# Performance work log

Measured on AMD Instinct MI355X. Metric: run time of the kernel, lower is better.

Reference implementation:

```python
import jax, jax.numpy as jnp
import numpy as np

D = 256
NH = 8
DH = D // NH
DFF = 1024
NLAYER = 6
LIN = 20
HOUT = 10
NEG = -1e9


def _ln(x, s, b, eps=1e-5):
    mu = jnp.mean(x, axis=-1, keepdims=True)
    var = jnp.mean((x - mu) ** 2, axis=-1, keepdims=True)
    return (x - mu) * jax.lax.rsqrt(var + eps) * s + b


def setup_inputs() -> dict:
    key = jax.random.key(0)
    ks = jax.random.split(key, 24)
    B, C, Q = 2, 1536, 512
    sc = 0.02
    inp = {
        'ctx_x': jax.random.normal(ks[0], (B, C, LIN), jnp.float32),
        'ctx_z': jax.random.normal(ks[1], (B, C, HOUT), jnp.float32),
        'qry_x': jax.random.normal(ks[2], (B, Q, LIN), jnp.float32),
        't_ctx': jax.random.randint(ks[3], (B, C), 0, 1024, jnp.int64 if jax.config.jax_enable_x64 else jnp.int32),
        't_qry': jax.random.randint(ks[4], (B, Q), 0, 2048, jnp.int64 if jax.config.jax_enable_x64 else jnp.int32),
        'W_ctx': sc * jax.random.normal(ks[5], (D, LIN + HOUT), jnp.float32),
        'b_ctx': jnp.zeros((D,), jnp.float32),
        'W_qry': sc * jax.random.normal(ks[6], (D, LIN + HOUT), jnp.float32),
        'b_qry': jnp.zeros((D,), jnp.float32),
        'alpha': 0.01 * jnp.ones((NH,), jnp.float32),
        'Wqkv': sc * jax.random.normal(ks[7], (NLAYER, 3 * D, D), jnp.float32),
        'bqkv': jnp.zeros((NLAYER, 3 * D), jnp.float32),
        'Wo': sc * jax.random.normal(ks[8], (NLAYER, D, D), jnp.float32),
        'bo': jnp.zeros((NLAYER, D), jnp.float32),
        'ln1_s': jnp.ones((NLAYER, D), jnp.float32),
        'ln1_b': jnp.zeros((NLAYER, D), jnp.float32),
        'W1': sc * jax.random.normal(ks[9], (NLAYER, DFF, D), jnp.float32),
        'b1': jnp.zeros((NLAYER, DFF), jnp.float32),
        'W2': sc * jax.random.normal(ks[10], (NLAYER, D, DFF), jnp.float32),
        'b2': jnp.zeros((NLAYER, D), jnp.float32),
        'ln2_s': jnp.ones((NLAYER, D), jnp.float32),
        'ln2_b': jnp.zeros((NLAYER, D), jnp.float32),
        'W_out': sc * jax.random.normal(ks[11], (HOUT, D), jnp.float32),
        'b_out': jnp.zeros((HOUT,), jnp.float32),
    }
    return inp


def _forward(ctx_x, ctx_z, qry_x, t_ctx, t_qry, W_ctx, b_ctx, W_qry, b_qry,
             alpha, Wqkv, bqkv, Wo, bo, ln1_s, ln1_b, W1, b1, W2, b2,
             ln2_s, ln2_b, W_out, b_out):
    B, C, _ = ctx_x.shape
    Q = qry_x.shape[1]
    S = C + Q
    ctx_in = jnp.concatenate([ctx_x, ctx_z], axis=-1)               # [B,C,L+H]
    qry_in = jnp.concatenate([qry_x, jnp.zeros((B, Q, HOUT), ctx_x.dtype)], axis=-1)
    Z = jnp.concatenate([ctx_in @ W_ctx.T + b_ctx,
                         qry_in @ W_qry.T + b_qry], axis=1)          # [B,S,d]
    t_all = jnp.concatenate([t_ctx, t_qry], axis=1)                  # [B,S]
    # structural mask: nobody attends to query columns (True = disallowed)
    struct = (jnp.arange(S)[None, :] >= C)                           # [1,S] -> broadcast over rows
    nofuture = t_all[:, :, None] < t_all[:, None, :]                 # [B,S,S]
    mask = struct[None, :, :] | nofuture                             # [B,S,S]
    # learnable per-head recency bias: -alpha_h * |t_i - t_j|
    dist = jnp.abs(t_all[:, :, None] - t_all[:, None, :]).astype(Z.dtype)
    bias = -alpha[None, :, None, None] * dist[:, None, :, :]         # [B,h,S,S]
    scale = 1.0 / np.sqrt(DH)

    for l in range(NLAYER):
        qkv = Z @ Wqkv[l].T + bqkv[l]                                # [B,S,3d]
        q, k, v = jnp.split(qkv, 3, axis=-1)
        q = q.reshape(B, S, NH, DH).transpose(0, 2, 1, 3)            # [B,h,S,dh]
        k = k.reshape(B, S, NH, DH).transpose(0, 2, 1, 3)
        v = v.reshape(B, S, NH, DH).transpose(0, 2, 1, 3)
        scores = jnp.einsum('bhid,bhjd->bhij', q, k) * scale + bias
        scores = jnp.where(mask[:, None, :, :], NEG, scores)
        p = jax.nn.softmax(scores, axis=-1)
        attn = jnp.einsum('bhij,bhjd->bhid', p, v)                   # [B,h,S,dh]
        attn = attn.transpose(0, 2, 1, 3).reshape(B, S, D)
        Z = _ln(Z + attn @ Wo[l].T + bo[l], ln1_s[l], ln1_b[l])
        ff = jax.nn.relu(Z @ W1[l].T + b1[l]) @ W2[l].T + b2[l]
        Z = _ln(Z + ff, ln2_s[l], ln2_b[l])

    return Z[:, C:, :] @ W_out.T + b_out                             # [B,Q,H]


def reference(ctx_x, ctx_z, qry_x, t_ctx, t_qry, W_ctx, b_ctx, W_qry, b_qry,
              alpha, Wqkv, bqkv, Wo, bo, ln1_s, ln1_b, W1, b1, W2, b2,
              ln2_s, ln2_b, W_out, b_out):
    return _forward(ctx_x, ctx_z, qry_x, t_ctx, t_qry, W_ctx, b_ctx, W_qry,
                    b_qry, alpha, Wqkv, bqkv, Wo, bo, ln1_s, ln1_b, W1, b1,
                    W2, b2, ln2_s, ln2_b, W_out, b_out)
```

## Files before the change

kernel.cpp:

```cpp
#include <hip/hip_runtime.h>
#include <hip/hip_bf16.h>
#include <cstddef>

#define BB   2
#define CTX  1536
#define QQ   512
#define S_LEN 2048
#define DD   256
#define NH   8
#define DH   32
#define DFF  1024
#define NL   6
#define LIN  20
#define HOUTD 10
#define KHALF (CTX / 2)

typedef _Float16 f16x2 __attribute__((ext_vector_type(2)));
typedef _Float16 f16x4 __attribute__((ext_vector_type(4)));
typedef _Float16 f16x8 __attribute__((ext_vector_type(8)));
typedef float f32x4 __attribute__((ext_vector_type(4)));

#define N4_QKV (NL * 3 * DD * DD / 4)
#define N4_WO  (NL * DD * DD / 4)
#define N4_W1  (NL * DFF * DD / 4)
#define N4_W2  (NL * DD * DFF / 4)

__global__ __launch_bounds__(256) void cvtall_k(
    const float* __restrict__ wqkv, const float* __restrict__ wo,
    const float* __restrict__ w1, const float* __restrict__ w2,
    _Float16* __restrict__ hqkv, _Float16* __restrict__ ho,
    _Float16* __restrict__ h1, _Float16* __restrict__ h2)
{
    int i = blockIdx.x * 256 + threadIdx.x;
    const float* s; _Float16* t; int j = i;
    if (j < N4_QKV) { s = wqkv; t = hqkv; }
    else if ((j -= N4_QKV) < N4_WO) { s = wo; t = ho; }
    else if ((j -= N4_WO) < N4_W1) { s = w1; t = h1; }
    else if ((j -= N4_W1) < N4_W2) { s = w2; t = h2; }
    else return;
    float4 v = ((const float4*)s)[j];
    f16x4 h = {(_Float16)v.x, (_Float16)v.y, (_Float16)v.z, (_Float16)v.w};
    ((f16x4*)t)[j] = h;
}

__global__ __launch_bounds__(256) void embed_k(
    const float* __restrict__ ctx_x, const float* __restrict__ ctx_z,
    const float* __restrict__ qry_x,
    const float* __restrict__ W_ctx, const float* __restrict__ b_ctx,
    const float* __restrict__ W_qry, const float* __restrict__ b_qry,
    const int* __restrict__ t_ctx, const int* __restrict__ t_qry,
    float* __restrict__ Z, _Float16* __restrict__ Zh, float* __restrict__ tf)
{
    int row = blockIdx.x;
    int d = threadIdx.x;
    int b = row >> 11, s = row & (S_LEN - 1);
    float acc;
    if (s < CTX) {
        const float* x1 = ctx_x + (size_t)(b * CTX + s) * LIN;
        const float* x2 = ctx_z + (size_t)(b * CTX + s) * HOUTD;
        const float* w = W_ctx + (size_t)d * (LIN + HOUTD);
        acc = b_ctx[d];
        #pragma unroll
        for (int i = 0; i < LIN; i++) acc += x1[i] * w[i];
        #pragma unroll
        for (int i = 0; i < HOUTD; i++) acc += x2[i] * w[LIN + i];
        if (d == 0) tf[row] = (float)t_ctx[b * CTX + s];
    } else {
        int qi = s - CTX;
        const float* x1 = qry_x + (size_t)(b * QQ + qi) * LIN;
        const float* w = W_qry + (size_t)d * (LIN + HOUTD);
        acc = b_qry[d];
        #pragma unroll
        for (int i = 0; i < LIN; i++) acc += x1[i] * w[i];
        if (d == 0) tf[row] = (float)t_qry[b * QQ + qi];
    }
    Z[(size_t)row * DD + d] = acc;
    Zh[(size_t)row * DD + d] = (_Float16)acc;
}

__global__ __launch_bounds__(256) void hgemm_k(
    const _Float16* __restrict__ X, const _Float16* __restrict__ W,
    const float* __restrict__ bias, float* __restrict__ Y,
    float* __restrict__ Ysplit, _Float16* __restrict__ Yh,
    int M, int N, int K, int lda, int mode,
    _Float16* __restrict__ Qh, _Float16* __restrict__ Kh, _Float16* __restrict__ Vh)
{
    __shared__ _Float16 Ah[2][64][40];
    __shared__ _Float16 Bh[2][64][40];
    const int tid = threadIdx.x;
    const int bm = blockIdx.x << 6, bn = blockIdx.y << 6;
    const int kbase = blockIdx.z * K;
    const int lr = tid >> 2;
    const int lk = (tid & 3) << 3;
    const int w = tid >> 6, lane = tid & 63;
    const int c = lane & 15, g = lane >> 4;
    const int wm = (w >> 1) << 5, wn = (w & 1) << 5;

    f32x4 acc00 = {0.f,0.f,0.f,0.f}, acc01 = {0.f,0.f,0.f,0.f};
    f32x4 acc10 = {0.f,0.f,0.f,0.f}, acc11 = {0.f,0.f,0.f,0.f};

    const _Float16* Xp = X + (size_t)(bm + lr) * lda + kbase + lk;
    const _Float16* Wp = W + (size_t)(bn + lr) * lda + kbase + lk;

    f16x8 xa = *(const f16x8*)Xp;
    f16x8 wb = *(const f16x8*)Wp;
    const int nt = K >> 5;
    int buf = 0;
    for (int t = 0; t < nt; t++) {
        *(f16x8*)&Ah[buf][lr][lk] = xa;
        *(f16x8*)&Bh[buf][lr][lk] = wb;
        __syncthreads();
        if (t + 1 < nt) {
            xa = *(const f16x8*)(Xp + ((size_t)(t + 1) << 5));
            wb = *(const f16x8*)(Wp + ((size_t)(t + 1) << 5));
        }
        f16x8 a0 = *(const f16x8*)&Ah[buf][wm + c][g << 3];
        f16x8 a1 = *(const f16x8*)&Ah[buf][wm + 16 + c][g << 3];
        f16x8 b0 = *(const f16x8*)&Bh[buf][wn + c][g << 3];
        f16x8 b1 = *(const f16x8*)&Bh[buf][wn + 16 + c][g << 3];
        acc00 = __builtin_amdgcn_mfma_f32_16x16x32_f16(a0, b0, acc00, 0, 0, 0);
        acc01 = __builtin_amdgcn_mfma_f32_16x16x32_f16(a0, b1, acc01, 0, 0, 0);
        acc10 = __builtin_amdgcn_mfma_f32_16x16x32_f16(a1, b0, acc10, 0, 0, 0);
        acc11 = __builtin_amdgcn_mfma_f32_16x16x32_f16(a1, b1, acc11, 0, 0, 0);
        buf ^= 1;
    }

    float* Yt = blockIdx.z ? Ysplit : Y;
    f32x4 accs[2][2] = {{acc00, acc01}, {acc10, acc11}};
    #pragma unroll
    for (int fm = 0; fm < 2; fm++) {
        #pragma unroll
        for (int fn = 0; fn < 2; fn++) {
            int colb = bn + wn + (fn << 4) + c;
            float bv = (blockIdx.z == 0) ? bias[colb] : 0.0f;
            #pragma unroll
            for (int r = 0; r < 4; r++) {
                int row = bm + wm + (fm << 4) + (g << 2) + r;
                float v = accs[fm][fn][r] + bv;
                if (mode == 0) {
                    Yt[(size_t)row * N + colb] = v;
                } else if (mode == 1) {
                    Yh[(size_t)row * N + colb] = (_Float16)fmaxf(v, 0.0f);
                } else {
                    int which = colb >> 8, h = (colb >> 5) & 7, d = colb & 31;
                    int bb2 = row >> 11, ss = row & (S_LEN - 1);
                    int bhi = (bb2 << 3) + h;
                    _Float16 hv = (_Float16)v;
                    if (which == 0)      Qh[((size_t)bhi * S_LEN + ss) * DH + d] = hv;
                    else if (which == 1) Kh[((size_t)bhi * S_LEN + ss) * DH + d] = hv;
                    else                 Vh[((size_t)bhi * DH + d) * S_LEN + ss] = hv;
                }
            }
        }
    }
}

__global__ __launch_bounds__(256) void gemmln_k(
    const _Float16* __restrict__ X, const _Float16* __restrict__ W,
    const float* __restrict__ bias, float* __restrict__ Z,
    _Float16* __restrict__ Zh, const float* __restrict__ sw,
    const float* __restrict__ bw)
{
    __shared__ _Float16 Ast[2][16][40];
    __shared__ _Float16 Bst[2][256][40];
    __shared__ float lred[4][16][2];
    const int tid = threadIdx.x;
    const int bm = blockIdx.x << 4;
    const int w = tid >> 6, lane = tid & 63;
    const int c = lane & 15, g = lane >> 4;
    const int br = tid >> 2, bk = (tid & 3) << 3;

    f32x4 acc[4] = {};
    const _Float16* Wp = W + (size_t)br * DD + bk;
    f16x8 p0 = *(const f16x8*)Wp;
    f16x8 p1 = *(const f16x8*)(Wp + (size_t)64 * DD);
    f16x8 p2 = *(const f16x8*)(Wp + (size_t)128 * DD);
    f16x8 p3 = *(const f16x8*)(Wp + (size_t)192 * DD);
    f16x8 xa;
    if (tid < 64) xa = *(const f16x8*)(X + (size_t)(bm + br) * DD + bk);
    int buf = 0;
    #pragma unroll
    for (int t = 0; t < 8; t++) {
        if (tid < 64) *(f16x8*)&Ast[buf][br][bk] = xa;
        *(f16x8*)&Bst[buf][br][bk] = p0;
        *(f16x8*)&Bst[buf][br + 64][bk] = p1;
        *(f16x8*)&Bst[buf][br + 128][bk] = p2;
        *(f16x8*)&Bst[buf][br + 192][bk] = p3;
        __syncthreads();
        if (t < 7) {
            int o = (t + 1) << 5;
            if (tid < 64) xa = *(const f16x8*)(X + (size_t)(bm + br) * DD + o + bk);
            p0 = *(const f16x8*)(Wp + o);
            p1 = *(const f16x8*)(Wp + (size_t)64 * DD + o);
            p2 = *(const f16x8*)(Wp + (size_t)128 * DD + o);
            p3 = *(const f16x8*)(Wp + (size_t)192 * DD + o);
        }
        f16x8 a = *(const f16x8*)&Ast[buf][c][g << 3];
        #pragma unroll
        for (int f = 0; f < 4; f++) {
            f16x8 bfr = *(const f16x8*)&Bst[buf][(w << 6) + (f << 4) + c][g << 3];
            acc[f] = __builtin_amdgcn_mfma_f32_16x16x32_f16(a, bfr, acc[f], 0, 0, 0);
        }
        buf ^= 1;
    }

    float vals[4][4];
    float s1[4] = {0.f,0.f,0.f,0.f}, s2[4] = {0.f,0.f,0.f,0.f};
    #pragma unroll
    for (int f = 0; f < 4; f++) {
        int col = (w << 6) + (f << 4) + c;
        float bv = bias[col];
        #pragma unroll
        for (int r = 0; r < 4; r++) {
            int row = bm + (g << 2) + r;
            float v = acc[f][r] + bv + Z[(size_t)row * DD + col];
            vals[f][r] = v; s1[r] += v; s2[r] += v * v;
        }
    }
    #pragma unroll
    for (int off = 1; off < 16; off <<= 1) {
        #pragma unroll
        for (int r = 0; r < 4; r++) {
            s1[r] += __shfl_xor(s1[r], off, 64);
            s2[r] += __shfl_xor(s2[r], off, 64);
        }
    }
    if (c == 0) {
        #pragma unroll
        for (int r = 0; r < 4; r++) {
            lred[w][(g << 2) + r][0] = s1[r];
            lred[w][(g << 2) + r][1] = s2[r];
        }
    }
    __syncthreads();
    float mu_r[4], rs_r[4];
    #pragma unroll
    for (int r = 0; r < 4; r++) {
        int lr_ = (g << 2) + r;
        float S1 = lred[0][lr_][0] + lred[1][lr_][0] + lred[2][lr_][0] + lred[3][lr_][0];
        float S2 = lred[0][lr_][1] + lred[1][lr_][1] + lred[2][lr_][1] + lred[3][lr_][1];
        float mu = S1 * (1.0f / 256.0f);
        float var = S2 * (1.0f / 256.0f) - mu * mu;
        mu_r[r] = mu; rs_r[r] = rsqrtf(var + 1e-5f);
    }
    #pragma unroll
    for (int f = 0; f < 4; f++) {
        int col = (w << 6) + (f << 4) + c;
        float swv = sw[col], bwv = bw[col];
        #pragma unroll
        for (int r = 0; r < 4; r++) {
            int row = bm + (g << 2) + r;
            float o = (vals[f][r] - mu_r[r]) * rs_r[r] * swv + bwv;
            Z[(size_t)row * DD + col] = o;
            Zh[(size_t)row * DD + col] = (_Float16)o;
        }
    }
}

__global__ __launch_bounds__(256) void ln4_k(
    float* __restrict__ Z, const float* __restrict__ Y0,
    const float* __restrict__ Y1,
    const float* __restrict__ sw, const float* __restrict__ bw,
    _Float16* __restrict__ Zh)
{
    const int w = threadIdx.x >> 6, lane = threadIdx.x & 63;
    const int row = (blockIdx.x << 2) + w;
    float4 z = ((const float4*)(Z + (size_t)row * DD))[lane];
    float4 y = ((const float4*)(Y0 + (size_t)row * DD))[lane];
    float4 y2 = ((const float4*)(Y1 + (size_t)row * DD))[lane];
    float x0 = z.x + y.x + y2.x, x1 = z.y + y.y + y2.y;
    float x2 = z.z + y.z + y2.z, x3 = z.w + y.w + y2.w;
    float s1 = (x0 + x1) + (x2 + x3);
    float s2 = (x0 * x0 + x1 * x1) + (x2 * x2 + x3 * x3);
    #pragma unroll
    for (int off = 1; off < 64; off <<= 1) {
        s1 += __shfl_xor(s1, off, 64);
        s2 += __shfl_xor(s2, off, 64);
    }
    float mu = s1 * (1.0f / 256.0f);
    float var = s2 * (1.0f / 256.0f) - mu * mu;
    float rs = rsqrtf(var + 1e-5f);
    float4 sv = ((const float4*)sw)[lane];
    float4 bv = ((const float4*)bw)[lane];
    float o0 = (x0 - mu) * rs * sv.x + bv.x;
    float o1 = (x1 - mu) * rs * sv.y + bv.y;
    float o2 = (x2 - mu) * rs * sv.z + bv.z;
    float o3 = (x3 - mu) * rs * sv.w + bv.w;
    ((float4*)(Z + (size_t)row * DD))[lane] = make_float4(o0, o1, o2, o3);
    f16x4 oh = {(_Float16)o0, (_Float16)o1, (_Float16)o2, (_Float16)o3};
    ((f16x4*)(Zh + (size_t)row * DD))[lane] = oh;
}

__global__ __launch_bounds__(1024, 4) void attn_k(
    const _Float16* __restrict__ Qf, const _Float16* __restrict__ Kf,
    const _Float16* __restrict__ Vf, const float* __restrict__ tf_all,
    const float* __restrict__ alpha, _Float16* __restrict__ O)
{
    const int bh = blockIdx.x >> 4;
    const int itile = blockIdx.x & 15;
    const int b = bh >> 3, h = bh & 7;
    const int tid = threadIdx.x;
    const int w16 = tid >> 6;
    const int wg = w16 >> 3;
    const int wq = w16 & 7;
    const int ltid = tid & 511;
    const int lane = tid & 63;
    const int c = lane & 15, g = lane >> 4;
    const int i0 = (itile << 7) + (wq << 4);
    const int jbase = wg * KHALF;

    __shared__ __align__(16) char smem[38912];
    _Float16 (*Kl)[2][64][40] = (_Float16(*)[2][64][40])smem;
    _Float16 (*Vl)[2][32][72] = (_Float16(*)[2][32][72])(smem + 20480);
    float (*sacc)[16][36] = (float(*)[16][36])smem;
    float (*sml)[2][16] = (float(*)[2][16])(smem + 36864);

    const float LOG2E = 1.44269504088896f;
    const float sc2 = 0.17677669529663687f * LOG2E;
    const float ah2 = alpha[h] * LOG2E;

    const _Float16* Qbh = Qf + (size_t)bh * S_LEN * DH;
    const _Float16* Kbh = Kf + (size_t)bh * S_LEN * DH;
    const _Float16* Vbh = Vf + (size_t)bh * DH * S_LEN;
    const float* tb = tf_all + b * S_LEN;

    f16x8 qfrag = *(const f16x8*)(Qbh + (size_t)(i0 + c) * DH + (g << 3));
    const float ti = tb[i0 + c];

    const int lh = ltid & 255;
    const int kr = lh >> 2, kc = (lh & 3) << 3;
    const int vr = lh >> 3, vc = (lh & 7) << 3;
    const bool doK = (ltid < 256);

    float m2 = -3.0e38f, l = 0.0f;
    f32x4 acc0 = {0.f, 0.f, 0.f, 0.f};
    f32x4 acc1 = {0.f, 0.f, 0.f, 0.f};
    const f32x4 zero = {0.f, 0.f, 0.f, 0.f};

    f16x8 pre;
    if (doK) pre = *(const f16x8*)(Kbh + (size_t)(jbase + kr) * DH + kc);
    else     pre = *(const f16x8*)(Vbh + (size_t)vr * S_LEN + jbase + vc);
    int buf = 0;

    for (int kt = 0; kt < KHALF; kt += 64) {
        if (doK) *(f16x8*)&Kl[wg][buf][kr][kc] = pre;
        else     *(f16x8*)&Vl[wg][buf][vr][vc] = pre;
        __syncthreads();
        if (kt + 64 < KHALF) {
            if (doK) pre = *(const f16x8*)(Kbh + (size_t)(jbase + kt + 64 + kr) * DH + kc);
            else     pre = *(const f16x8*)(Vbh + (size_t)vr * S_LEN + jbase + kt + 64 + vc);
        }
        #pragma unroll
        for (int jj = 0; jj < 64; jj += 32) {
            const int j0 = jbase + kt + jj;
            f16x8 kf0 = *(const f16x8*)&Kl[wg][buf][jj + c][g << 3];
            f16x8 kf1 = *(const f16x8*)&Kl[wg][buf][jj + 16 + c][g << 3];
            f32x4 dA = __builtin_amdgcn_mfma_f32_16x16x32_f16(kf0, qfrag, zero, 0, 0, 0);
            f32x4 dB = __builtin_amdgcn_mfma_f32_16x16x32_f16(kf1, qfrag, zero, 0, 0, 0);
            float4 tjA = *(const float4*)(tb + j0 + (g << 2));
            float4 tjB = *(const float4*)(tb + j0 + 16 + (g << 2));
            float eA0 = ti - tjA.x, eA1 = ti - tjA.y, eA2 = ti - tjA.z, eA3 = ti - tjA.w;
            float eB0 = ti - tjB.x, eB1 = ti - tjB.y, eB2 = ti - tjB.z, eB3 = ti - tjB.w;
            float sA0 = (eA0 >= 0.f) ? dA[0] * sc2 - ah2 * eA0 : -1e9f;
            float sA1 = (eA1 >= 0.f) ? dA[1] * sc2 - ah2 * eA1 : -1e9f;
            float sA2 = (eA2 >= 0.f) ? dA[2] * sc2 - ah2 * eA2 : -1e9f;
            float sA3 = (eA3 >= 0.f) ? dA[3] * sc2 - ah2 * eA3 : -1e9f;
            float sB0 = (eB0 >= 0.f) ? dB[0] * sc2 - ah2 * eB0 : -1e9f;
            float sB1 = (eB1 >= 0.f) ? dB[1] * sc2 - ah2 * eB1 : -1e9f;
            float sB2 = (eB2 >= 0.f) ? dB[2] * sc2 - ah2 * eB2 : -1e9f;
            float sB3 = (eB3 >= 0.f) ? dB[3] * sc2 - ah2 * eB3 : -1e9f;
            float pmaxl = fmaxf(fmaxf(fmaxf(sA0, sA1), fmaxf(sA2, sA3)),
                                fmaxf(fmaxf(sB0, sB1), fmaxf(sB2, sB3)));
            if (__any(pmaxl > m2 + 8.0f)) {
                float pm = fmaxf(pmaxl, __shfl_xor(pmaxl, 16, 64));
                pm = fmaxf(pm, __shfl_xor(pm, 32, 64));
                float mnew = fmaxf(m2, pm);
                float fsc = __builtin_amdgcn_exp2f(m2 - mnew);
                m2 = mnew;
                l *= fsc; acc0 *= fsc; acc1 *= fsc;
            }
            float pA0 = __builtin_amdgcn_exp2f(sA0 - m2);
            float pA1 = __builtin_amdgcn_exp2f(sA1 - m2);
            float pA2 = __builtin_amdgcn_exp2f(sA2 - m2);
            float pA3 = __builtin_amdgcn_exp2f(sA3 - m2);
            float pB0 = __builtin_amdgcn_exp2f(sB0 - m2);
            float pB1 = __builtin_amdgcn_exp2f(sB1 - m2);
            float pB2 = __builtin_amdgcn_exp2f(sB2 - m2);
            float pB3 = __builtin_amdgcn_exp2f(sB3 - m2);
            l += ((pA0 + pA1) + (pA2 + pA3)) + ((pB0 + pB1) + (pB2 + pB3));
            f16x4 pfA = {(_Float16)pA0, (_Float16)pA1, (_Float16)pA2, (_Float16)pA3};
            f16x4 pfB = {(_Float16)pB0, (_Float16)pB1, (_Float16)pB2, (_Float16)pB3};
            f16x4 vA0 = *(const f16x4*)&Vl[wg][buf][c][jj + (g << 2)];
            f16x4 vA1 = *(const f16x4*)&Vl[wg][buf][16 + c][jj + (g << 2)];
            f16x4 vB0 = *(const f16x4*)&Vl[wg][buf][c][jj + 16 + (g << 2)];
            f16x4 vB1 = *(const f16x4*)&Vl[wg][buf][16 + c][jj + 16 + (g << 2)];
            acc0 = __builtin_amdgcn_mfma_f32_16x16x16f16(vA0, pfA, acc0, 0, 0, 0);
            acc0 = __builtin_amdgcn_mfma_f32_16x16x16f16(vB0, pfB, acc0, 0, 0, 0);
            acc1 = __builtin_amdgcn_mfma_f32_16x16x16f16(vA1, pfA, acc1, 0, 0, 0);
            acc1 = __builtin_amdgcn_mfma_f32_16x16x16f16(vB1, pfB, acc1, 0, 0, 0);
        }
        buf ^= 1;
    }

    l += __shfl_xor(l, 16, 64);
    l += __shfl_xor(l, 32, 64);

    __syncthreads();
    *(f32x4*)&sacc[w16][c][g << 2] = acc0;
    *(f32x4*)&sacc[w16][c][16 + (g << 2)] = acc1;
    if (g == 0) { sml[w16][0][c] = m2; sml[w16][1][c] = l; }
    __syncthreads();

    {
        const int qt = tid >> 7;
        const int q = (tid >> 3) & 15;
        const int dh0 = (tid & 7) << 2;
        float m0 = sml[qt][0][q], m1 = sml[qt + 8][0][q];
        float M = fmaxf(m0, m1);
        float f0 = __builtin_amdgcn_exp2f(m0 - M);
        float f1 = __builtin_amdgcn_exp2f(m1 - M);
        float L = sml[qt][1][q] * f0 + sml[qt + 8][1][q] * f1;
        float a0 = sacc[qt][q][dh0 + 0] * f0 + sacc[qt + 8][q][dh0 + 0] * f1;
        float a1 = sacc[qt][q][dh0 + 1] * f0 + sacc[qt + 8][q][dh0 + 1] * f1;
        float a2 = sacc[qt][q][dh0 + 2] * f0 + sacc[qt + 8][q][dh0 + 2] * f1;
        float a3 = sacc[qt][q][dh0 + 3] * f0 + sacc[qt + 8][q][dh0 + 3] * f1;
        if (M < -4.9e8f) {
            float vs0 = 0.f, vs1 = 0.f, vs2 = 0.f, vs3 = 0.f;
            const _Float16* vp = Vbh + (size_t)dh0 * S_LEN + CTX;
            for (int j = 0; j < QQ; j += 8) {
                f16x8 x0 = *(const f16x8*)(vp + j);
                f16x8 x1 = *(const f16x8*)(vp + S_LEN + j);
                f16x8 x2 = *(const f16x8*)(vp + 2 * S_LEN + j);
                f16x8 x3 = *(const f16x8*)(vp + 3 * S_LEN + j);
                #pragma unroll
                for (int e = 0; e < 8; e++) {
                    vs0 += (float)x0[e]; vs1 += (float)x1[e];
                    vs2 += (float)x2[e]; vs3 += (float)x3[e];
                }
            }
            a0 += vs0; a1 += vs1; a2 += vs2; a3 += vs3;
            L += (float)QQ;
        }
        float inv = 1.0f / L;
        int row = b * S_LEN + (itile << 7) + (qt << 4) + q;
        f16x4 o = {(_Float16)(a0 * inv), (_Float16)(a1 * inv),
                   (_Float16)(a2 * inv), (_Float16)(a3 * inv)};
        *(f16x4*)(O + (size_t)row * DD + h * DH + dh0) = o;
    }
}

__global__ __launch_bounds__(256) void outhead_k(
    const float* __restrict__ Z, const float* __restrict__ Wout,
    const float* __restrict__ bout, float* __restrict__ out)
{
    int tid = threadIdx.x;
    int rloc = tid >> 4, ho = tid & 15;
    int qrow = blockIdx.x * 16 + rloc;
    int b = qrow >> 9, qi = qrow & (QQ - 1);
    if (ho < HOUTD) {
        const float* z = Z + (size_t)(b * S_LEN + CTX + qi) * DD;
        const float* wr = Wout + (size_t)ho * DD;
        float s = 0.0f;
        for (int d = 0; d < DD; d += 4) {
            float4 zv = *(const float4*)(z + d);
            float4 wv = *(const float4*)(wr + d);
            s += zv.x * wv.x + zv.y * wv.y + zv.z * wv.z + zv.w * wv.w;
        }
        out[(size_t)(b * QQ + qi) * HOUTD + ho] = s + bout[ho];
    }
}

extern "C" void kernel_launch(void* const* d_in, const int* in_sizes, int n_in,
                              void* d_out, int out_size, void* d_ws, size_t ws_size,
                              hipStream_t stream) {
    (void)in_sizes; (void)n_in; (void)out_size; (void)ws_size;
    const float* ctx_x = (const float*)d_in[0];
    const float* ctx_z = (const float*)d_in[1];
    const float* qry_x = (const float*)d_in[2];
    const int* t_ctx = (const int*)d_in[3];
    const int* t_qry = (const int*)d_in[4];
    const float* W_ctx = (const float*)d_in[5];
    const float* b_ctx = (const float*)d_in[6];
    const float* W_qry = (const float*)d_in[7];
    const float* b_qry = (const float*)d_in[8];
    const float* alpha = (const float*)d_in[9];
    const float* Wqkv = (const float*)d_in[10];
    const float* bqkv = (const float*)d_in[11];
    const float* Wo = (const float*)d_in[12];
    const float* bo = (const float*)d_in[13];
    const float* ln1_s = (const float*)d_in[14];
    const float* ln1_b = (const float*)d_in[15];
    const float* W1 = (const float*)d_in[16];
    const float* b1 = (const float*)d_in[17];
    const float* W2 = (const float*)d_in[18];
    const float* b2 = (const float*)d_in[19];
    const float* ln2_s = (const float*)d_in[20];
    const float* ln2_b = (const float*)d_in[21];
    const float* W_out = (const float*)d_in[22];
    const float* b_out = (const float*)d_in[23];

    float* ws = (float*)d_ws;
    const size_t MTOT = (size_t)BB * S_LEN;
    const size_t ZSZ = MTOT * DD;
    float* Z   = ws;
    float* Yb  = ws + ZSZ;
    _Float16* Zh   = (_Float16*)(ws + 2 * ZSZ);
    _Float16* AYh  = (_Float16*)(ws + 2 * ZSZ + ZSZ / 2);
    _Float16* FF1h = (_Float16*)(ws + 3 * ZSZ);
    _Float16* Qh   = (_Float16*)(ws + 5 * ZSZ);
    _Float16* Kh   = (_Float16*)(ws + 5 * ZSZ + ZSZ / 2);
    _Float16* Vh   = (_Float16*)(ws + 6 * ZSZ);
    float* Yb1 = ws + 5 * ZSZ;
    float* tf_all  = ws + 6 * ZSZ + ZSZ / 2;
    _Float16* Whqkv = (_Float16*)(ws + 6 * ZSZ + ZSZ / 2 + 4096);
    _Float16* Who   = Whqkv + (size_t)NL * 3 * DD * DD;
    _Float16* Wh1   = Who   + (size_t)NL * DD * DD;
    _Float16* Wh2   = Wh1   + (size_t)NL * DFF * DD;

    {
        int n4tot = N4_QKV + N4_WO + N4_W1 + N4_W2;
        cvtall_k<<<(n4tot + 255) / 256, 256, 0, stream>>>(
            Wqkv, Wo, W1, W2, Whqkv, Who, Wh1, Wh2);
    }

    embed_k<<<MTOT, 256, 0, stream>>>(ctx_x, ctx_z, qry_x, W_ctx, b_ctx, W_qry, b_qry,
                                      t_ctx, t_qry, Z, Zh, tf_all);

    for (int l = 0; l < NL; l++) {
        hgemm_k<<<dim3(MTOT / 64, (3 * DD) / 64, 1), 256, 0, stream>>>(
            Zh, Whqkv + (size_t)l * 3 * DD * DD, bqkv + (size_t)l * 3 * DD,
            nullptr, nullptr, nullptr, (int)MTOT, 3 * DD, DD, DD, 2, Qh, Kh, Vh);
        attn_k<<<BB * NH * (S_LEN / 128), 1024, 0, stream>>>(
            Qh, Kh, Vh, tf_all, alpha, AYh);
        gemmln_k<<<MTOT / 16, 256, 0, stream>>>(
            AYh, Who + (size_t)l * DD * DD, bo + (size_t)l * DD,
            Z, Zh, ln1_s + (size_t)l * DD, ln1_b + (size_t)l * DD);
        hgemm_k<<<dim3(MTOT / 64, DFF / 64, 1), 256, 0, stream>>>(
            Zh, Wh1 + (size_t)l * DFF * DD, b1 + (size_t)l * DFF,
            nullptr, nullptr, FF1h, (int)MTOT, DFF, DD, DD, 1,
            nullptr, nullptr, nullptr);
        hgemm_k<<<dim3(MTOT / 64, DD / 64, 2), 256, 0, stream>>>(
            FF1h, Wh2 + (size_t)l * DD * DFF, b2 + (size_t)l * DD,
            Yb, Yb1, nullptr, (int)MTOT, DD, DFF / 2, DFF, 0,
            nullptr, nullptr, nullptr);
        ln4_k<<<MTOT / 4, 256, 0, stream>>>(
            Z, Yb, Yb1, ln2_s + (size_t)l * DD, ln2_b + (size_t)l * DD, Zh);
    }

    outhead_k<<<(BB * QQ) / 16, 256, 0, stream>>>(Z, W_out, b_out, (float*)d_out);
}
```

Before: 439.1 us.

## Widen attention K/V tiles to 128, cache times in LDS, split FFN2 four ways

The attention kernel now stages 128-key K and V tiles per iteration, with every thread loading both K and V. This halves the number of barriers and loop trips. The per-batch time vector is also copied into shared memory, so the inner loop reads it from LDS instead of global memory. The second FFN GEMM goes from a 2-way to a 4-way split-K to fill more of the GPU, and the layernorm kernel sums four partial outputs. The costs are much more LDS per attention block (about 84KB), which may limit occupancy, plus extra partial-buffer traffic in the FFN and layernorm.

```diff
diff --git a/kernel.cpp b/kernel.cpp
--- a/kernel.cpp
+++ b/kernel.cpp
@@ -80,8 +80,9 @@
 
 __global__ __launch_bounds__(256) void hgemm_k(
     const _Float16* __restrict__ X, const _Float16* __restrict__ W,
-    const float* __restrict__ bias, float* __restrict__ Y,
-    float* __restrict__ Ysplit, _Float16* __restrict__ Yh,
+    const float* __restrict__ bias, float* __restrict__ Y0,
+    float* __restrict__ Y1, float* __restrict__ Y2, float* __restrict__ Y3,
+    _Float16* __restrict__ Yh,
     int M, int N, int K, int lda, int mode,
     _Float16* __restrict__ Qh, _Float16* __restrict__ Kh, _Float16* __restrict__ Vh)
 {
@@ -125,7 +126,8 @@
         buf ^= 1;
     }
 
-    float* Yt = blockIdx.z ? Ysplit : Y;
+    float* Yt = (blockIdx.z == 0) ? Y0 : (blockIdx.z == 1) ? Y1
+              : (blockIdx.z == 2) ? Y2 : Y3;
     f32x4 accs[2][2] = {{acc00, acc01}, {acc10, acc11}};
     #pragma unroll
     for (int fm = 0; fm < 2; fm++) {
@@ -259,17 +261,22 @@
 
 __global__ __launch_bounds__(256) void ln4_k(
     float* __restrict__ Z, const float* __restrict__ Y0,
-    const float* __restrict__ Y1,
+    const float* __restrict__ Y1, const float* __restrict__ Y2,
+    const float* __restrict__ Y3,
     const float* __restrict__ sw, const float* __restrict__ bw,
     _Float16* __restrict__ Zh)
 {
     const int w = threadIdx.x >> 6, lane = threadIdx.x & 63;
     const int row = (blockIdx.x << 2) + w;
     float4 z = ((const float4*)(Z + (size_t)row * DD))[lane];
-    float4 y = ((const float4*)(Y0 + (size_t)row * DD))[lane];
-    float4 y2 = ((const float4*)(Y1 + (size_t)row * DD))[lane];
-    float x0 = z.x + y.x + y2.x, x1 = z.y + y.y + y2.y;
-    float x2 = z.z + y.z + y2.z, x3 = z.w + y.w + y2.w;
+    float4 y0 = ((const float4*)(Y0 + (size_t)row * DD))[lane];
+    float4 y1 = ((const float4*)(Y1 + (size_t)row * DD))[lane];
+    float4 y2 = ((const float4*)(Y2 + (size_t)row * DD))[lane];
+    float4 y3 = ((const float4*)(Y3 + (size_t)row * DD))[lane];
+    float x0 = z.x + (y0.x + y1.x) + (y2.x + y3.x);
+    float x1 = z.y + (y0.y + y1.y) + (y2.y + y3.y);
+    float x2 = z.z + (y0.z + y1.z) + (y2.z + y3.z);
+    float x3 = z.w + (y0.w + y1.w) + (y2.w + y3.w);
     float s1 = (x0 + x1) + (x2 + x3);
     float s2 = (x0 * x0 + x1 * x1) + (x2 * x2 + x3 * x3);
     #pragma unroll
@@ -309,9 +316,10 @@
     const int i0 = (itile << 7) + (wq << 4);
     const int jbase = wg * KHALF;
 
-    __shared__ __align__(16) char smem[38912];
-    _Float16 (*Kl)[2][64][40] = (_Float16(*)[2][64][40])smem;
-    _Float16 (*Vl)[2][32][72] = (_Float16(*)[2][32][72])(smem + 20480);
+    __shared__ __align__(16) char smem[83968];
+    _Float16 (*Kl)[2][128][40] = (_Float16(*)[2][128][40])smem;
+    _Float16 (*Vl)[2][32][136] = (_Float16(*)[2][32][136])(smem + 40960);
+    float* tbl = (float*)(smem + 75776);
     float (*sacc)[16][36] = (float(*)[16][36])smem;
     float (*sml)[2][16] = (float(*)[2][16])(smem + 36864);
 
@@ -327,38 +335,38 @@
     f16x8 qfrag = *(const f16x8*)(Qbh + (size_t)(i0 + c) * DH + (g << 3));
     const float ti = tb[i0 + c];
 
-    const int lh = ltid & 255;
-    const int kr = lh >> 2, kc = (lh & 3) << 3;
-    const int vr = lh >> 3, vc = (lh & 7) << 3;
-    const bool doK = (ltid < 256);
+    const int kr = ltid >> 2, kc = (ltid & 3) << 3;
+    const int vr = ltid >> 4, vc = (ltid & 15) << 3;
+
+    tbl[tid] = tb[tid];
+    tbl[tid + 1024] = tb[tid + 1024];
 
     float m2 = -3.0e38f, l = 0.0f;
     f32x4 acc0 = {0.f, 0.f, 0.f, 0.f};
     f32x4 acc1 = {0.f, 0.f, 0.f, 0.f};
     const f32x4 zero = {0.f, 0.f, 0.f, 0.f};
 
-    f16x8 pre;
-    if (doK) pre = *(const f16x8*)(Kbh + (size_t)(jbase + kr) * DH + kc);
-    else     pre = *(const f16x8*)(Vbh + (size_t)vr * S_LEN + jbase + vc);
+    f16x8 kpre = *(const f16x8*)(Kbh + (size_t)(jbase + kr) * DH + kc);
+    f16x8 vpre = *(const f16x8*)(Vbh + (size_t)vr * S_LEN + jbase + vc);
     int buf = 0;
 
-    for (int kt = 0; kt < KHALF; kt += 64) {
-        if (doK) *(f16x8*)&Kl[wg][buf][kr][kc] = pre;
-        else     *(f16x8*)&Vl[wg][buf][vr][vc] = pre;
+    for (int kt = 0; kt < KHALF; kt += 128) {
+        *(f16x8*)&Kl[wg][buf][kr][kc] = kpre;
+        *(f16x8*)&Vl[wg][buf][vr][vc] = vpre;
         __syncthreads();
-        if (kt + 64 < KHALF) {
-            if (doK) pre = *(const f16x8*)(Kbh + (size_t)(jbase + kt + 64 + kr) * DH + kc);
-            else     pre = *(const f16x8*)(Vbh + (size_t)vr * S_LEN + jbase + kt + 64 + vc);
-        }
-        #pragma unroll
-        for (int jj = 0; jj < 64; jj += 32) {
+        if (kt + 128 < KHALF) {
+            kpre = *(const f16x8*)(Kbh + (size_t)(jbase + kt + 128 + kr) * DH + kc);
+            vpre = *(const f16x8*)(Vbh + (size_t)vr * S_LEN + jbase + kt + 128 + vc);
+        }
+        #pragma unroll
+        for (int jj = 0; jj < 128; jj += 32) {
             const int j0 = jbase + kt + jj;
             f16x8 kf0 = *(const f16x8*)&Kl[wg][buf][jj + c][g << 3];
             f16x8 kf1 = *(const f16x8*)&Kl[wg][buf][jj + 16 + c][g << 3];
             f32x4 dA = __builtin_amdgcn_mfma_f32_16x16x32_f16(kf0, qfrag, zero, 0, 0, 0);
             f32x4 dB = __builtin_amdgcn_mfma_f32_16x16x32_f16(kf1, qfrag, zero, 0, 0, 0);
-            float4 tjA = *(const float4*)(tb + j0 + (g << 2));
-            float4 tjB = *(const float4*)(tb + j0 + 16 + (g << 2));
+            float4 tjA = *(const float4*)&tbl[j0 + (g << 2)];
+            float4 tjB = *(const float4*)&tbl[j0 + 16 + (g << 2)];
             float eA0 = ti - tjA.x, eA1 = ti - tjA.y, eA2 = ti - tjA.z, eA3 = ti - tjA.w;
             float eB0 = ti - tjB.x, eB1 = ti - tjB.y, eB2 = ti - tjB.z, eB3 = ti - tjB.w;
             float sA0 = (eA0 >= 0.f) ? dA[0] * sc2 - ah2 * eA0 : -1e9f;
@@ -510,12 +518,14 @@
     _Float16* Qh   = (_Float16*)(ws + 5 * ZSZ);
     _Float16* Kh   = (_Float16*)(ws + 5 * ZSZ + ZSZ / 2);
     _Float16* Vh   = (_Float16*)(ws + 6 * ZSZ);
-    float* Yb1 = ws + 5 * ZSZ;
     float* tf_all  = ws + 6 * ZSZ + ZSZ / 2;
     _Float16* Whqkv = (_Float16*)(ws + 6 * ZSZ + ZSZ / 2 + 4096);
     _Float16* Who   = Whqkv + (size_t)NL * 3 * DD * DD;
     _Float16* Wh1   = Who   + (size_t)NL * DD * DD;
     _Float16* Wh2   = Wh1   + (size_t)NL * DFF * DD;
+    float* Yb1 = ws + 9 * ZSZ;
+    float* Yb2 = ws + 10 * ZSZ;
+    float* Yb3 = ws + 11 * ZSZ;
 
     {
         int n4tot = N4_QKV + N4_WO + N4_W1 + N4_W2;
@@ -529,7 +539,8 @@
     for (int l = 0; l < NL; l++) {
         hgemm_k<<<dim3(MTOT / 64, (3 * DD) / 64, 1), 256, 0, stream>>>(
             Zh, Whqkv + (size_t)l * 3 * DD * DD, bqkv + (size_t)l * 3 * DD,
-            nullptr, nullptr, nullptr, (int)MTOT, 3 * DD, DD, DD, 2, Qh, Kh, Vh);
+            nullptr, nullptr, nullptr, nullptr, nullptr,
+            (int)MTOT, 3 * DD, DD, DD, 2, Qh, Kh, Vh);
         attn_k<<<BB * NH * (S_LEN / 128), 1024, 0, stream>>>(
             Qh, Kh, Vh, tf_all, alpha, AYh);
         gemmln_k<<<MTOT / 16, 256, 0, stream>>>(
@@ -537,14 +548,15 @@
             Z, Zh, ln1_s + (size_t)l * DD, ln1_b + (size_t)l * DD);
         hgemm_k<<<dim3(MTOT / 64, DFF / 64, 1), 256, 0, stream>>>(
             Zh, Wh1 + (size_t)l * DFF * DD, b1 + (size_t)l * DFF,
-            nullptr, nullptr, FF1h, (int)MTOT, DFF, DD, DD, 1,
-            nullptr, nullptr, nullptr);
-        hgemm_k<<<dim3(MTOT / 64, DD / 64, 2), 256, 0, stream>>>(
+            nullptr, nullptr, nullptr, nullptr, FF1h,
+            (int)MTOT, DFF, DD, DD, 1, nullptr, nullptr, nullptr);
+        hgemm_k<<<dim3(MTOT / 64, DD / 64, 4), 256, 0, stream>>>(
             FF1h, Wh2 + (size_t)l * DD * DFF, b2 + (size_t)l * DD,
-            Yb, Yb1, nullptr, (int)MTOT, DD, DFF / 2, DFF, 0,
-            nullptr, nullptr, nullptr);
+            Yb, Yb1, Yb2, Yb3, nullptr,
+            (int)MTOT, DD, DFF / 4, DFF, 0, nullptr, nullptr, nullptr);
         ln4_k<<<MTOT / 4, 256, 0, stream>>>(
-            Z, Yb, Yb1, ln2_s + (size_t)l * DD, ln2_b + (size_t)l * DD, Zh);
+            Z, Yb, Yb1, Yb2, Yb3,
+            ln2_s + (size_t)l * DD, ln2_b + (size_t)l * DD, Zh);
     }
 
     outhead_k<<<(BB * QQ) / 16, 256, 0, stream>>>(Z, W_out, b_out, (float*)d_out);
```

Result: faster. 423.3 us (-3.6%).
